# Kernel optimization log

Measured on AMD Instinct MI355X. Metric: run time of the kernel, lower is better.

The kernel has to match this reference:

```python
import jax, jax.numpy as jnp
import numpy as np

B, L, E, H, DV, V = 256, 512, 200, 256, 30000, 50000
NEG_INF = -jnp.inf

def setup_inputs() -> dict:
    key = jax.random.key(0)
    ks = jax.random.split(key, 16)
    s = 0.05
    f = jnp.float32
    return {
        "input_id": jax.random.randint(ks[0], (B, 1), 0, V),
        "input_emb": jax.random.normal(ks[1], (B, 1, E), f),
        "encoder_outputs": jax.random.normal(ks[2], (B, L, H), f),
        "encoder_input_ids": jax.random.randint(ks[3], (B, L), 0, V),
        "hidden": jax.random.normal(ks[4], (B, 1, H), f),
        "attention": jax.random.normal(ks[5], (B, 1, H), f),
        # GRU (PyTorch layout): W_ih (3H, 2H+E), W_hh (3H, H), gate order r,z,n
        "W_ih": jax.random.normal(ks[6], (3 * H, 2 * H + E), f) * s,
        "W_hh": jax.random.normal(ks[7], (3 * H, H), f) * s,
        "b_ih": jnp.zeros((3 * H,), f),
        "b_hh": jnp.zeros((3 * H,), f),
        "W_attn": jax.random.normal(ks[8], (H, H), f) * s,
        "b_attn": jnp.zeros((H,), f),
        "W_comb": jax.random.normal(ks[9], (H, 2 * H), f) * s,
        "b_comb": jnp.zeros((H,), f),
        "W_gen": jax.random.normal(ks[10], (DV, H), f) * s,
        "b_gen": jnp.zeros((DV,), f),
        "W_copy": jax.random.normal(ks[11], (H, H), f) * s,
        "b_copy": jnp.zeros((H,), f),
    }


def reference(input_id, input_emb, encoder_outputs, encoder_input_ids, hidden,
              attention, W_ih, W_hh, b_ih, b_hh, W_attn, b_attn, W_comb,
              b_comb, W_gen, b_gen, W_copy, b_copy):
    b, l = encoder_input_ids.shape
    # selective read: rou = normalized match mask (NaN guard -> 0)
    mask = (input_id == encoder_input_ids).astype(encoder_outputs.dtype)  # (b,l)
    msum = jnp.sum(mask, axis=1, keepdims=True)
    rou = jnp.where(msum > 0, mask / jnp.where(msum > 0, msum, 1.0), 0.0)
    selective_read = jnp.einsum('bl,blh->bh', rou, encoder_outputs)  # (b,h)

    # GRU single step (dropout is identity at inference)
    x = jnp.concatenate([input_emb[:, 0], attention[:, 0], selective_read], axis=-1)
    h_prev = hidden[:, 0]  # (b,h)
    gx = x @ W_ih.T + b_ih          # (b,3h)
    gh = h_prev @ W_hh.T + b_hh     # (b,3h)
    xr, xz, xn = jnp.split(gx, 3, axis=-1)
    hr, hz, hn = jnp.split(gh, 3, axis=-1)
    r = jax.nn.sigmoid(xr + hr)
    z = jax.nn.sigmoid(xz + hz)
    n = jnp.tanh(xn + r * hn)
    h = (1.0 - z) * n + z * h_prev  # (b,h) cur_hidden

    # attention
    q = h @ W_attn.T + b_attn
    attn_w = jax.nn.softmax(jnp.einsum('bh,blh->bl', q, encoder_outputs), axis=-1)
    attn_applied = jnp.einsum('bl,blh->bh', attn_w, encoder_outputs)
    cur_attention = jnp.tanh(
        jnp.concatenate([attn_applied, h], axis=-1) @ W_comb.T + b_comb)  # (b,h)

    # generate + copy scores, joint softmax
    generate_score = cur_attention @ W_gen.T + b_gen                     # (b,DV)
    copy_weights = jax.nn.sigmoid(encoder_outputs @ W_copy.T + b_copy)   # (b,l,h)
    copy_score = jnp.einsum('blh,bh->bl', copy_weights, cur_attention)   # (b,l)
    score = jax.nn.softmax(jnp.concatenate([generate_score, copy_score], axis=1), axis=1)
    gen_s, copy_s = score[:, :DV], score[:, DV:]

    # fused equivalent of the one-hot scatter/mix: direct scatter-add into vocab
    output = jnp.zeros((b, V), score.dtype)
    output = output.at[:, :DV].add(gen_s)
    output = output.at[jnp.arange(b)[:, None], encoder_input_ids].add(copy_s)

    pos = output > 0
    out = jnp.where(pos, jnp.log(jnp.where(pos, output, 1.0)), NEG_INF)
    return out, h[:, None, :], cur_attention[:, None, :]
```

## Files before the change

kernel.cpp:

```cpp
#include <hip/hip_runtime.h>
#include <cmath>

#define B_  256
#define L_  512
#define E_  200
#define H_  256
#define DV_ 30000
#define V_  50000
#define X_  712
#define G3_ 768

#define NEG_BIG -1.0e30f

typedef __attribute__((ext_vector_type(8))) _Float16 half8;
typedef __attribute__((ext_vector_type(4))) float   floatx4;

#define GLOAD16(gptr, lptr)                                                            \
    __builtin_amdgcn_global_load_lds(                                                  \
        (const __attribute__((address_space(1))) unsigned int*)(gptr),                 \
        (__attribute__((address_space(3))) unsigned int*)(lptr), 16, 0, 0)

__global__ void k_cast_wc(const float* __restrict__ Wc, _Float16* __restrict__ wcb) {
    int i = blockIdx.x * 256 + threadIdx.x;
    wcb[i] = (_Float16)Wc[i];
}

__global__ void k_selread(const int* __restrict__ input_id, const float* __restrict__ emb,
                          const float* __restrict__ attention, const float* __restrict__ hidden,
                          const float* __restrict__ enc, const int* __restrict__ enc_ids,
                          float* __restrict__ xT) {
    int b = blockIdx.x, t = threadIdx.x;
    __shared__ int cnt;
    __shared__ int list[L_];
    if (t == 0) cnt = 0;
    __syncthreads();
    int id = input_id[b];
    for (int l = t; l < L_; l += 256) {
        if (enc_ids[b * L_ + l] == id) { int p = atomicAdd(&cnt, 1); list[p] = l; }
    }
    __syncthreads();
    int n = cnt;
    float s = 0.f;
    for (int i = 0; i < n; i++) s += enc[(b * L_ + list[i]) * H_ + t];
    float sel = (n > 0) ? s / (float)n : 0.f;
    for (int k = t; k < E_; k += 256) xT[k * B_ + b] = emb[b * E_ + k];
    xT[(E_ + t) * B_ + b]       = attention[b * H_ + t];
    xT[(E_ + H_ + t) * B_ + b]  = sel;
    xT[(X_ + t) * B_ + b]       = hidden[b * H_ + t];
}

template<int K>
__global__ void __launch_bounds__(256) k_gru_one(const float* __restrict__ xTp, const float* __restrict__ W,
                                                 const float* __restrict__ bias, float* __restrict__ g) {
    __shared__ __align__(16) float Ws[8 * K];
    int t  = threadIdx.x;
    int j0 = blockIdx.x * 8;
    int bq = t & 63;
    int jh = t >> 6;
#pragma unroll
    for (int jj = 0; jj < 8; jj++) {
        const float4* src = (const float4*)(W + (size_t)(j0 + jj) * K);
        float4* dst = (float4*)(Ws + jj * K);
        for (int i = t; i < K / 4; i += 256) dst[i] = src[i];
    }
    __syncthreads();
    float acc0[4] = {0.f, 0.f, 0.f, 0.f};
    float acc1[4] = {0.f, 0.f, 0.f, 0.f};
    const float* w0 = Ws + (jh * 2 + 0) * K;
    const float* w1 = Ws + (jh * 2 + 1) * K;
#pragma unroll 2
    for (int k4 = 0; k4 < K / 4; k4++) {
        float4 wa = *(const float4*)(w0 + k4 * 4);
        float4 wb = *(const float4*)(w1 + k4 * 4);
        float wav[4] = {wa.x, wa.y, wa.z, wa.w};
        float wbv[4] = {wb.x, wb.y, wb.z, wb.w};
#pragma unroll
        for (int u = 0; u < 4; u++) {
            float4 xv = *(const float4*)(xTp + (size_t)(k4 * 4 + u) * B_ + bq * 4);
            acc0[0] += wav[u] * xv.x; acc0[1] += wav[u] * xv.y;
            acc0[2] += wav[u] * xv.z; acc0[3] += wav[u] * xv.w;
            acc1[0] += wbv[u] * xv.x; acc1[1] += wbv[u] * xv.y;
            acc1[2] += wbv[u] * xv.z; acc1[3] += wbv[u] * xv.w;
        }
    }
    int ja = j0 + jh * 2, jb = ja + 1;
    float ba = bias[ja], bb = bias[jb];
#pragma unroll
    for (int i = 0; i < 4; i++) {
        g[(size_t)(bq * 4 + i) * G3_ + ja] = acc0[i] + ba;
        g[(size_t)(bq * 4 + i) * G3_ + jb] = acc1[i] + bb;
    }
}

__global__ void k_gru_gates(const float* __restrict__ gx, const float* __restrict__ gh,
                            const float* __restrict__ hidden, float* __restrict__ hws,
                            float* __restrict__ hout) {
    int b = blockIdx.x, j = threadIdx.x;
    float xr = gx[b * G3_ + j], xz = gx[b * G3_ + 256 + j], xn = gx[b * G3_ + 512 + j];
    float hr = gh[b * G3_ + j], hz = gh[b * G3_ + 256 + j], hn = gh[b * G3_ + 512 + j];
    float r = 1.f / (1.f + expf(-(xr + hr)));
    float z = 1.f / (1.f + expf(-(xz + hz)));
    float n = tanhf(xn + r * hn);
    float hp = hidden[b * H_ + j];
    float h = (1.f - z) * n + z * hp;
    hws[b * H_ + j] = h;
    hout[b * H_ + j] = h;
}

__global__ void __launch_bounds__(1024) k_attn(const float* __restrict__ hws, const float* __restrict__ enc,
                       const float* __restrict__ W_attn, const float* __restrict__ b_attn,
                       const float* __restrict__ W_comb, const float* __restrict__ b_comb,
                       float* __restrict__ caws, _Float16* __restrict__ cab,
                       float* __restrict__ caout) {
    int b = blockIdx.x, t = threadIdx.x;
    int lane = t & 63, w = t >> 6;
    int jj = t & 255, ph = t >> 8;
    __shared__ float hs[H_], qs[H_], ap[H_];
    __shared__ float part[16][H_];
    __shared__ float rm[16], rd[16];
    if (t < 256) hs[t] = hws[b * H_ + t];
    __syncthreads();
    {
        const float4* wr = (const float4*)(W_attn + (size_t)jj * H_ + ph * 64);
        const float4* hp = (const float4*)(hs + ph * 64);
        float acc = 0.f;
#pragma unroll
        for (int k4 = 0; k4 < 16; k4++) {
            float4 wv = wr[k4]; float4 hv = hp[k4];
            acc += wv.x * hv.x + wv.y * hv.y + wv.z * hv.z + wv.w * hv.w;
        }
        part[ph][jj] = acc;
    }
    __syncthreads();
    if (t < 256) qs[t] = b_attn[t] + part[0][t] + part[1][t] + part[2][t] + part[3][t];
    __syncthreads();
    {
        float4 q4 = *(const float4*)&qs[lane * 4];
        size_t base = (size_t)b * L_ + w * 32;
        float m = -INFINITY, d = 0.f;
        float ax = 0.f, ay = 0.f, az = 0.f, aw = 0.f;
        for (int i = 0; i < 32; i += 8) {
            float4 e[8];
            float s[8];
#pragma unroll
            for (int u = 0; u < 8; u++) {
                e[u] = *(const float4*)(enc + (base + i + u) * H_ + lane * 4);
                s[u] = q4.x * e[u].x + q4.y * e[u].y + q4.z * e[u].z + q4.w * e[u].w;
            }
#pragma unroll
            for (int u = 0; u < 8; u++) {
#pragma unroll
                for (int o = 1; o < 64; o <<= 1) s[u] += __shfl_xor(s[u], o);
            }
#pragma unroll
            for (int u = 0; u < 8; u++) {
                float mn = fmaxf(m, s[u]);
                float fm = __expf(m - mn);
                float fs = __expf(s[u] - mn);
                d  = d  * fm + fs;
                ax = ax * fm + fs * e[u].x;
                ay = ay * fm + fs * e[u].y;
                az = az * fm + fs * e[u].z;
                aw = aw * fm + fs * e[u].w;
                m = mn;
            }
        }
        float* pw = &part[w][lane * 4];
        pw[0] = ax; pw[1] = ay; pw[2] = az; pw[3] = aw;
        if (lane == 0) { rm[w] = m; rd[w] = d; }
    }
    __syncthreads();
    if (t < 256) {
        float M = rm[0];
#pragma unroll
        for (int i = 1; i < 16; i++) M = fmaxf(M, rm[i]);
        float den = 0.f, num = 0.f;
#pragma unroll
        for (int i = 0; i < 16; i++) {
            float f = __expf(rm[i] - M);
            den += rd[i] * f;
            num += part[i][t] * f;
        }
        ap[t] = num / den;
    }
    __syncthreads();
    {
        const float4* wr = (const float4*)(W_comb + (size_t)jj * (2 * H_) + ph * 128);
        const float4* xp = (const float4*)(((ph & 2) ? hs : ap) + (ph & 1) * 128);
        float acc = 0.f;
#pragma unroll
        for (int k4 = 0; k4 < 32; k4++) {
            float4 wv = wr[k4]; float4 xv = xp[k4];
            acc += wv.x * xv.x + wv.y * xv.y + wv.z * xv.z + wv.w * xv.w;
        }
        part[ph][jj] = acc;
    }
    __syncthreads();
    if (t < 256) {
        float cav = tanhf(b_comb[t] + part[0][t] + part[1][t] + part[2][t] + part[3][t]);
        caws[b * H_ + t] = cav;
        cab[b * H_ + t]  = (_Float16)cav;
        caout[b * H_ + t] = cav;
    }
}

__global__ void __launch_bounds__(256, 2) k_gen_mfma(
        const _Float16* __restrict__ cab, const float* __restrict__ W_gen,
        const float* __restrict__ b_gen, float* __restrict__ out) {
    __shared__ __align__(16) _Float16 Ah[128 * 32];
    __shared__ __align__(16) float    Bf[128 * 32];
    int t = threadIdx.x, w = t >> 6, lane = t & 63;
    int n0 = blockIdx.x * 128, m0 = blockIdx.y * 128;
    int wm = (w >> 1) * 64, wn = (w & 1) * 64;
    int l15 = lane & 15, q = lane >> 4;
    floatx4 acc[4][4];
#pragma unroll
    for (int i = 0; i < 4; i++)
#pragma unroll
        for (int j = 0; j < 4; j++) acc[i][j] = (floatx4){0.f, 0.f, 0.f, 0.f};

    for (int kc = 0; kc < H_; kc += 32) {
#pragma unroll
        for (int i = 0; i < 2; i++) {
            int t2 = w * 2 + i;
            int row = t2 * 16 + (lane >> 2);
            const _Float16* g = cab + (size_t)(m0 + row) * H_ + kc + (lane & 3) * 8;
            GLOAD16(g, &Ah[t2 * 512]);
        }
#pragma unroll
        for (int i = 0; i < 4; i++) {
            int t2 = w * 4 + i;
            int row = t2 * 8 + (lane >> 3);
            int nn = n0 + row; nn = nn < DV_ ? nn : DV_ - 1;
            const float* g = W_gen + (size_t)nn * H_ + kc + (lane & 7) * 4;
            GLOAD16(g, &Bf[t2 * 256]);
        }
        __syncthreads();
        half8 a[4];
#pragma unroll
        for (int mi = 0; mi < 4; mi++) {
            int m = wm + mi * 16 + l15;
            a[mi] = *(const half8*)&Ah[m * 32 + q * 8];
        }
#pragma unroll
        for (int ni = 0; ni < 4; ni++) {
            int n = wn + ni * 16 + l15;
            const float4* bp = (const float4*)&Bf[n * 32 + q * 8];
            float4 f0 = bp[0], f1 = bp[1];
            half8 bf;
            bf[0] = (_Float16)f0.x; bf[1] = (_Float16)f0.y; bf[2] = (_Float16)f0.z; bf[3] = (_Float16)f0.w;
            bf[4] = (_Float16)f1.x; bf[5] = (_Float16)f1.y; bf[6] = (_Float16)f1.z; bf[7] = (_Float16)f1.w;
#pragma unroll
            for (int mi = 0; mi < 4; mi++)
                acc[mi][ni] = __builtin_amdgcn_mfma_f32_16x16x32_f16(a[mi], bf, acc[mi][ni], 0, 0, 0);
        }
        __syncthreads();
    }
#pragma unroll
    for (int ni = 0; ni < 4; ni++) {
        int col = n0 + wn + ni * 16 + l15;
        if (col < DV_) {
            float bg = b_gen[col];
#pragma unroll
            for (int mi = 0; mi < 4; mi++)
#pragma unroll
                for (int j = 0; j < 4; j++) {
                    int row = m0 + wm + mi * 16 + q * 4 + j;
                    out[(size_t)row * V_ + col] = acc[mi][ni][j] + bg;
                }
        }
    }
}

__global__ void __launch_bounds__(256, 2) k_copy_mfma(
        const float* __restrict__ enc, const _Float16* __restrict__ wcb,
        const float* __restrict__ b_copy, const float* __restrict__ caws,
        float* __restrict__ copy_s) {
    __shared__ __align__(16) float    Af[128 * 32];
    __shared__ __align__(16) _Float16 Bh[256 * 32];
    __shared__ float bcs[H_], cas[H_];
    int t = threadIdx.x, w = t >> 6, lane = t & 63;
    int R0 = blockIdx.x * 128;
    int b  = blockIdx.x >> 2;
    int l15 = lane & 15, q = lane >> 4;
    bcs[t] = b_copy[t];
    cas[t] = caws[b * H_ + t];
    floatx4 acc[2][16];
#pragma unroll
    for (int i = 0; i < 2; i++)
#pragma unroll
        for (int j = 0; j < 16; j++) acc[i][j] = (floatx4){0.f, 0.f, 0.f, 0.f};

    for (int kc = 0; kc < H_; kc += 32) {
#pragma unroll
        for (int i = 0; i < 4; i++) {
            int t2 = w * 4 + i;
            int row = t2 * 8 + (lane >> 3);
            const float* g = enc + (size_t)(R0 + row) * H_ + kc + (lane & 7) * 4;
            GLOAD16(g, &Af[t2 * 256]);
        }
#pragma unroll
        for (int i = 0; i < 4; i++) {
            int t2 = w * 4 + i;
            int row = t2 * 16 + (lane >> 2);
            const _Float16* g = wcb + row * H_ + kc + (lane & 3) * 8;
            GLOAD16(g, &Bh[t2 * 512]);
        }
        __syncthreads();
        half8 a[2];
#pragma unroll
        for (int mi = 0; mi < 2; mi++) {
            int m = w * 32 + mi * 16 + l15;
            const float4* apx = (const float4*)&Af[m * 32 + q * 8];
            float4 f0 = apx[0], f1 = apx[1];
            half8 h;
            h[0] = (_Float16)f0.x; h[1] = (_Float16)f0.y; h[2] = (_Float16)f0.z; h[3] = (_Float16)f0.w;
            h[4] = (_Float16)f1.x; h[5] = (_Float16)f1.y; h[6] = (_Float16)f1.z; h[7] = (_Float16)f1.w;
            a[mi] = h;
        }
#pragma unroll
        for (int ni = 0; ni < 16; ni++) {
            int n = ni * 16 + l15;
            half8 bf = *(const half8*)&Bh[n * 32 + q * 8];
            acc[0][ni] = __builtin_amdgcn_mfma_f32_16x16x32_f16(a[0], bf, acc[0][ni], 0, 0, 0);
            acc[1][ni] = __builtin_amdgcn_mfma_f32_16x16x32_f16(a[1], bf, acc[1][ni], 0, 0, 0);
        }
        __syncthreads();
    }
#pragma unroll
    for (int mi = 0; mi < 2; mi++) {
#pragma unroll
        for (int j = 0; j < 4; j++) {
            float p = 0.f;
#pragma unroll
            for (int ni = 0; ni < 16; ni++) {
                int col = ni * 16 + l15;
                float v = acc[mi][ni][j] + bcs[col];
                p += cas[col] / (1.f + __expf(-v));
            }
            p += __shfl_xor(p, 1);
            p += __shfl_xor(p, 2);
            p += __shfl_xor(p, 4);
            p += __shfl_xor(p, 8);
            if (l15 == 0) copy_s[R0 + w * 32 + mi * 16 + q * 4 + j] = p;
        }
    }
}

__global__ void __launch_bounds__(1024) k_stats(const float* __restrict__ out, const float* __restrict__ copy_s,
                        float* __restrict__ mrow, float* __restrict__ ldrow) {
    int b = blockIdx.x, t = threadIdx.x, lane = t & 63, w = t >> 6;
    __shared__ float rm[16], rs[16];
    const float* row = out + (size_t)b * V_;
    float m = -INFINITY, s = 0.f;
    for (int j = t; j < DV_; j += 1024) {
        float v = row[j];
        if (v > m) { s = s * __expf(m - v) + 1.f; m = v; }
        else       s += __expf(v - m);
    }
    if (t < 512) {
        float v = copy_s[b * L_ + t];
        if (v > m) { s = s * __expf(m - v) + 1.f; m = v; }
        else       s += __expf(v - m);
    }
#pragma unroll
    for (int o = 1; o < 64; o <<= 1) {
        float m2 = __shfl_xor(m, o), s2 = __shfl_xor(s, o);
        float mn = fmaxf(m, m2);
        s = s * __expf(m - mn) + s2 * __expf(m2 - mn);
        m = mn;
    }
    if (lane == 0) { rm[w] = m; rs[w] = s; }
    __syncthreads();
    if (t == 0) {
        float M = rm[0], S = rs[0];
        for (int i = 1; i < 16; i++) {
            float mn = fmaxf(M, rm[i]);
            S = S * __expf(M - mn) + rs[i] * __expf(rm[i] - mn);
            M = mn;
        }
        mrow[b] = M;
        ldrow[b] = __logf(S);
    }
}

__global__ void __launch_bounds__(1024) k_final(float* __restrict__ out, const float* __restrict__ mrow,
                        const float* __restrict__ ldrow) {
    int j = blockIdx.x * 1024 + threadIdx.x;
    int b = blockIdx.y;
    if (j >= V_) return;
    size_t idx = (size_t)b * V_ + j;
    float sh = mrow[b] + ldrow[b];
    out[idx] = (j < DV_) ? out[idx] - sh : NEG_BIG;
}

__global__ void k_scatter_log(float* __restrict__ out, const float* __restrict__ copy_s,
                              const int* __restrict__ enc_ids, const float* __restrict__ mrow,
                              const float* __restrict__ ldrow) {
    int l = blockIdx.x * 256 + threadIdx.x;
    int b = blockIdx.y;
    float p = __expf(copy_s[b * L_ + l] - mrow[b] - ldrow[b]);
    unsigned int* up = (unsigned int*)(out + (size_t)b * V_ + enc_ids[b * L_ + l]);
    unsigned int cur = *up;
    while (true) {
        float ov = __uint_as_float(cur);
        float pv = (ov < -1.0e29f) ? p : __expf(ov) + p;
        unsigned int prev = atomicCAS(up, cur, __float_as_uint(__logf(pv)));
        if (prev == cur) break;
        cur = prev;
    }
}

extern "C" void kernel_launch(void* const* d_in, const int* in_sizes, int n_in,
                              void* d_out, int out_size, void* d_ws, size_t ws_size,
                              hipStream_t stream) {
    const int*   input_id  = (const int*)  d_in[0];
    const float* input_emb = (const float*)d_in[1];
    const float* enc       = (const float*)d_in[2];
    const int*   enc_ids   = (const int*)  d_in[3];
    const float* hidden    = (const float*)d_in[4];
    const float* attention = (const float*)d_in[5];
    const float* W_ih      = (const float*)d_in[6];
    const float* W_hh      = (const float*)d_in[7];
    const float* b_ih      = (const float*)d_in[8];
    const float* b_hh      = (const float*)d_in[9];
    const float* W_attn    = (const float*)d_in[10];
    const float* b_attn    = (const float*)d_in[11];
    const float* W_comb    = (const float*)d_in[12];
    const float* b_comb    = (const float*)d_in[13];
    const float* W_gen     = (const float*)d_in[14];
    const float* b_gen     = (const float*)d_in[15];
    const float* W_copy    = (const float*)d_in[16];
    const float* b_copy    = (const float*)d_in[17];

    float* out = (float*)d_out;
    float* ws  = (float*)d_ws;
    float* xT   = ws;
    float* gx   = xT + 247808;
    float* gh   = gx + 196608;
    float* hws  = gh + 196608;
    float* caws = hws + 65536;
    float* cps  = caws + 65536;
    float* mrow = cps + 131072;
    float* ldrow = mrow + 256;
    _Float16* wcb = (_Float16*)(ldrow + 256);
    _Float16* cab = wcb + 65536;

    float* hout  = out + (size_t)B_ * V_;
    float* caout = hout + B_ * H_;

    k_cast_wc<<<256, 256, 0, stream>>>(W_copy, wcb);
    k_selread<<<256, 256, 0, stream>>>(input_id, input_emb, attention, hidden, enc, enc_ids, xT);
    k_gru_one<712><<<96, 256, 0, stream>>>(xT, W_ih, b_ih, gx);
    k_gru_one<256><<<96, 256, 0, stream>>>(xT + X_ * B_, W_hh, b_hh, gh);
    k_gru_gates<<<256, 256, 0, stream>>>(gx, gh, hidden, hws, hout);
    k_attn<<<256, 1024, 0, stream>>>(hws, enc, W_attn, b_attn, W_comb, b_comb, caws, cab, caout);
    k_gen_mfma<<<dim3((DV_ + 127) / 128, 2), 256, 0, stream>>>(cab, W_gen, b_gen, out);
    k_copy_mfma<<<(B_ * L_) / 128, 256, 0, stream>>>(enc, wcb, b_copy, caws, cps);
    k_stats<<<256, 1024, 0, stream>>>(out, cps, mrow, ldrow);
    dim3 gf((V_ + 1023) / 1024, B_);
    k_final<<<gf, 1024, 0, stream>>>(out, mrow, ldrow);
    dim3 gs(L_ / 256, B_);
    k_scatter_log<<<gs, 256, 0, stream>>>(out, cps, enc_ids, mrow, ldrow);
}
```

Measured before the change: 488.1 us.

## Double-buffer encoder chunks in LDS with block-wide online softmax in attention

```diff
diff --git a/kernel.cpp b/kernel.cpp
--- a/kernel.cpp
+++ b/kernel.cpp
@@ -107,6 +107,7 @@
     hout[b * H_ + j] = h;
 }
 
+#define CHUNK_ 64
 __global__ void __launch_bounds__(1024) k_attn(const float* __restrict__ hws, const float* __restrict__ enc,
                        const float* __restrict__ W_attn, const float* __restrict__ b_attn,
                        const float* __restrict__ W_comb, const float* __restrict__ b_comb,
@@ -115,11 +116,22 @@
     int b = blockIdx.x, t = threadIdx.x;
     int lane = t & 63, w = t >> 6;
     int jj = t & 255, ph = t >> 8;
+    __shared__ __align__(16) float buf[2][CHUNK_ * H_];
     __shared__ float hs[H_], qs[H_], ap[H_];
-    __shared__ float part[16][H_];
-    __shared__ float rm[16], rd[16];
+    __shared__ float part[4][H_];
+    __shared__ float sc[CHUNK_], ps[CHUNK_];
+    __shared__ float mS, dS, fS;
+    const float* encb = enc + (size_t)b * (L_ * H_);
+
+#pragma unroll
+    for (int i = 0; i < 4; i++) {
+        int rs = w * 4 + i;
+        GLOAD16(encb + rs * H_ + lane * 4, &buf[0][rs * H_]);
+    }
     if (t < 256) hs[t] = hws[b * H_ + t];
-    __syncthreads();
+    if (t == 0) { mS = -INFINITY; dS = 0.f; }
+    __syncthreads();
+
     {
         const float4* wr = (const float4*)(W_attn + (size_t)jj * H_ + ph * 64);
         const float4* hp = (const float4*)(hs + ph * 64);
@@ -134,56 +146,64 @@
     __syncthreads();
     if (t < 256) qs[t] = b_attn[t] + part[0][t] + part[1][t] + part[2][t] + part[3][t];
     __syncthreads();
-    {
-        float4 q4 = *(const float4*)&qs[lane * 4];
-        size_t base = (size_t)b * L_ + w * 32;
-        float m = -INFINITY, d = 0.f;
-        float ax = 0.f, ay = 0.f, az = 0.f, aw = 0.f;
-        for (int i = 0; i < 32; i += 8) {
-            float4 e[8];
-            float s[8];
-#pragma unroll
-            for (int u = 0; u < 8; u++) {
-                e[u] = *(const float4*)(enc + (base + i + u) * H_ + lane * 4);
-                s[u] = q4.x * e[u].x + q4.y * e[u].y + q4.z * e[u].z + q4.w * e[u].w;
+
+    float4 q4 = *(const float4*)&qs[lane * 4];
+    float apacc = 0.f;
+    int cur = 0;
+    for (int c = 0; c < L_ / CHUNK_; c++) {
+        if (c < L_ / CHUNK_ - 1) {
+            const float* src = encb + (size_t)(c + 1) * (CHUNK_ * H_);
+#pragma unroll
+            for (int i = 0; i < 4; i++) {
+                int rs = w * 4 + i;
+                GLOAD16(src + rs * H_ + lane * 4, &buf[cur ^ 1][rs * H_]);
             }
-#pragma unroll
-            for (int u = 0; u < 8; u++) {
-#pragma unroll
-                for (int o = 1; o < 64; o <<= 1) s[u] += __shfl_xor(s[u], o);
+        }
+#pragma unroll
+        for (int i = 0; i < 4; i++) {
+            int r = w * 4 + i;
+            float4 e = *(const float4*)&buf[cur][r * H_ + lane * 4];
+            float s = q4.x * e.x + q4.y * e.y + q4.z * e.z + q4.w * e.w;
+#pragma unroll
+            for (int o = 1; o < 64; o <<= 1) s += __shfl_xor(s, o);
+            if (lane == 0) sc[r] = s;
+        }
+        __syncthreads();
+        if (w == 0) {
+            float v = sc[lane];
+            float mc = v;
+#pragma unroll
+            for (int o = 1; o < 64; o <<= 1) mc = fmaxf(mc, __shfl_xor(mc, o));
+            float mold = mS;
+            float mnew = fmaxf(mold, mc);
+            float p = __expf(v - mnew);
+            ps[lane] = p;
+            float dsum = p;
+#pragma unroll
+            for (int o = 1; o < 64; o <<= 1) dsum += __shfl_xor(dsum, o);
+            if (lane == 0) {
+                float f = __expf(mold - mnew);
+                fS = f;
+                dS = dS * f + dsum;
+                mS = mnew;
             }
-#pragma unroll
-            for (int u = 0; u < 8; u++) {
-                float mn = fmaxf(m, s[u]);
-                float fm = __expf(m - mn);
-                float fs = __expf(s[u] - mn);
-                d  = d  * fm + fs;
-                ax = ax * fm + fs * e[u].x;
-                ay = ay * fm + fs * e[u].y;
-                az = az * fm + fs * e[u].z;
-                aw = aw * fm + fs * e[u].w;
-                m = mn;
-            }
-        }
-        float* pw = &part[w][lane * 4];
-        pw[0] = ax; pw[1] = ay; pw[2] = az; pw[3] = aw;
-        if (lane == 0) { rm[w] = m; rd[w] = d; }
-    }
-    __syncthreads();
-    if (t < 256) {
-        float M = rm[0];
-#pragma unroll
-        for (int i = 1; i < 16; i++) M = fmaxf(M, rm[i]);
-        float den = 0.f, num = 0.f;
-#pragma unroll
-        for (int i = 0; i < 16; i++) {
-            float f = __expf(rm[i] - M);
-            den += rd[i] * f;
-            num += part[i][t] * f;
-        }
-        ap[t] = num / den;
-    }
-    __syncthreads();
+        }
+        __syncthreads();
+        {
+            float f = fS;
+            apacc *= f;
+            const float* bp = &buf[cur][ph * 16 * H_ + jj];
+#pragma unroll
+            for (int r = 0; r < 16; r++) apacc += ps[ph * 16 + r] * bp[r * H_];
+        }
+        __syncthreads();
+        cur ^= 1;
+    }
+    part[ph][jj] = apacc;
+    __syncthreads();
+    if (t < 256) ap[t] = (part[0][t] + part[1][t] + part[2][t] + part[3][t]) / dS;
+    __syncthreads();
+
     {
         const float4* wr = (const float4*)(W_comb + (size_t)jj * (2 * H_) + ph * 128);
         const float4* xp = (const float4*)(((ph & 2) ? hs : ap) + (ph & 1) * 128);
```

Result: faster. 477.2 us (-2.2%).

## Split attention kernel into query GEMM, chunked softmax, and combine stages

Applied to the files above, without the earlier changes.

```diff
diff --git a/kernel.cpp b/kernel.cpp
--- a/kernel.cpp
+++ b/kernel.cpp
@@ -49,7 +49,7 @@
     xT[(X_ + t) * B_ + b]       = hidden[b * H_ + t];
 }
 
-template<int K>
+template<int K, int OS>
 __global__ void __launch_bounds__(256) k_gru_one(const float* __restrict__ xTp, const float* __restrict__ W,
                                                  const float* __restrict__ bias, float* __restrict__ g) {
     __shared__ __align__(16) float Ws[8 * K];
@@ -87,14 +87,14 @@
     float ba = bias[ja], bb = bias[jb];
 #pragma unroll
     for (int i = 0; i < 4; i++) {
-        g[(size_t)(bq * 4 + i) * G3_ + ja] = acc0[i] + ba;
-        g[(size_t)(bq * 4 + i) * G3_ + jb] = acc1[i] + bb;
+        g[(size_t)(bq * 4 + i) * OS + ja] = acc0[i] + ba;
+        g[(size_t)(bq * 4 + i) * OS + jb] = acc1[i] + bb;
     }
 }
 
 __global__ void k_gru_gates(const float* __restrict__ gx, const float* __restrict__ gh,
                             const float* __restrict__ hidden, float* __restrict__ hws,
-                            float* __restrict__ hout) {
+                            float* __restrict__ hT, float* __restrict__ hout) {
     int b = blockIdx.x, j = threadIdx.x;
     float xr = gx[b * G3_ + j], xz = gx[b * G3_ + 256 + j], xn = gx[b * G3_ + 512 + j];
     float hr = gh[b * G3_ + j], hz = gh[b * G3_ + 256 + j], hn = gh[b * G3_ + 512 + j];
@@ -104,104 +104,100 @@
     float hp = hidden[b * H_ + j];
     float h = (1.f - z) * n + z * hp;
     hws[b * H_ + j] = h;
+    hT[j * B_ + b]  = h;
     hout[b * H_ + j] = h;
 }
 
-__global__ void __launch_bounds__(1024) k_attn(const float* __restrict__ hws, const float* __restrict__ enc,
-                       const float* __restrict__ W_attn, const float* __restrict__ b_attn,
-                       const float* __restrict__ W_comb, const float* __restrict__ b_comb,
-                       float* __restrict__ caws, _Float16* __restrict__ cab,
-                       float* __restrict__ caout) {
+#define NC_ 4
+#define CR_ 128
+__global__ void __launch_bounds__(256) k_attn_a(const float* __restrict__ qws, const float* __restrict__ enc,
+                         float* __restrict__ avp, float* __restrict__ mdp) {
+    int blk = blockIdx.x;
+    int b = blk >> 2, c = blk & 3;
+    int t = threadIdx.x, lane = t & 63, w = t >> 6;
+    __shared__ float ps[CR_];
+    __shared__ float red[8];
+    const float* encc = enc + ((size_t)b * L_ + c * CR_) * H_;
+    float4 q4 = *(const float4*)&qws[b * H_ + lane * 4];
+    for (int i = 0; i < 32; i += 8) {
+        float s[8];
+#pragma unroll
+        for (int u = 0; u < 8; u++) {
+            float4 e = *(const float4*)(encc + (size_t)(w * 32 + i + u) * H_ + lane * 4);
+            s[u] = q4.x * e.x + q4.y * e.y + q4.z * e.z + q4.w * e.w;
+        }
+#pragma unroll
+        for (int u = 0; u < 8; u++) {
+#pragma unroll
+            for (int o = 1; o < 64; o <<= 1) s[u] += __shfl_xor(s[u], o);
+            if (lane == 0) ps[w * 32 + i + u] = s[u];
+        }
+    }
+    __syncthreads();
+    {
+        float v = ps[w * 32 + (lane & 31)];
+#pragma unroll
+        for (int o = 1; o < 64; o <<= 1) v = fmaxf(v, __shfl_xor(v, o));
+        if (lane == 0) red[w] = v;
+    }
+    __syncthreads();
+    float M = fmaxf(fmaxf(red[0], red[1]), fmaxf(red[2], red[3]));
+    float e = (t < CR_) ? __expf(ps[t] - M) : 0.f;
+    {
+        float ssum = e;
+#pragma unroll
+        for (int o = 1; o < 64; o <<= 1) ssum += __shfl_xor(ssum, o);
+        if (lane == 0) red[4 + w] = ssum;
+    }
+    __syncthreads();
+    if (t < CR_) ps[t] = e;
+    if (t == 0) {
+        mdp[blk * 2]     = M;
+        mdp[blk * 2 + 1] = red[4] + red[5] + red[6] + red[7];
+    }
+    __syncthreads();
+    float a0 = 0.f, a1 = 0.f, a2 = 0.f, a3 = 0.f;
+#pragma unroll 4
+    for (int r = 0; r < CR_; r += 4) {
+        a0 += ps[r + 0] * encc[(size_t)(r + 0) * H_ + t];
+        a1 += ps[r + 1] * encc[(size_t)(r + 1) * H_ + t];
+        a2 += ps[r + 2] * encc[(size_t)(r + 2) * H_ + t];
+        a3 += ps[r + 3] * encc[(size_t)(r + 3) * H_ + t];
+    }
+    avp[(size_t)blk * H_ + t] = (a0 + a1) + (a2 + a3);
+}
+
+__global__ void __launch_bounds__(256) k_attn_b(const float* __restrict__ avp, const float* __restrict__ mdp,
+                         const float* __restrict__ hws, const float* __restrict__ W_comb,
+                         const float* __restrict__ b_comb,
+                         float* __restrict__ caws, _Float16* __restrict__ cab,
+                         float* __restrict__ caout) {
     int b = blockIdx.x, t = threadIdx.x;
-    int lane = t & 63, w = t >> 6;
-    int jj = t & 255, ph = t >> 8;
-    __shared__ float hs[H_], qs[H_], ap[H_];
-    __shared__ float part[16][H_];
-    __shared__ float rm[16], rd[16];
-    if (t < 256) hs[t] = hws[b * H_ + t];
-    __syncthreads();
-    {
-        const float4* wr = (const float4*)(W_attn + (size_t)jj * H_ + ph * 64);
-        const float4* hp = (const float4*)(hs + ph * 64);
-        float acc = 0.f;
-#pragma unroll
-        for (int k4 = 0; k4 < 16; k4++) {
-            float4 wv = wr[k4]; float4 hv = hp[k4];
-            acc += wv.x * hv.x + wv.y * hv.y + wv.z * hv.z + wv.w * hv.w;
-        }
-        part[ph][jj] = acc;
-    }
-    __syncthreads();
-    if (t < 256) qs[t] = b_attn[t] + part[0][t] + part[1][t] + part[2][t] + part[3][t];
-    __syncthreads();
-    {
-        float4 q4 = *(const float4*)&qs[lane * 4];
-        size_t base = (size_t)b * L_ + w * 32;
-        float m = -INFINITY, d = 0.f;
-        float ax = 0.f, ay = 0.f, az = 0.f, aw = 0.f;
-        for (int i = 0; i < 32; i += 8) {
-            float4 e[8];
-            float s[8];
-#pragma unroll
-            for (int u = 0; u < 8; u++) {
-                e[u] = *(const float4*)(enc + (base + i + u) * H_ + lane * 4);
-                s[u] = q4.x * e[u].x + q4.y * e[u].y + q4.z * e[u].z + q4.w * e[u].w;
-            }
-#pragma unroll
-            for (int u = 0; u < 8; u++) {
-#pragma unroll
-                for (int o = 1; o < 64; o <<= 1) s[u] += __shfl_xor(s[u], o);
-            }
-#pragma unroll
-            for (int u = 0; u < 8; u++) {
-                float mn = fmaxf(m, s[u]);
-                float fm = __expf(m - mn);
-                float fs = __expf(s[u] - mn);
-                d  = d  * fm + fs;
-                ax = ax * fm + fs * e[u].x;
-                ay = ay * fm + fs * e[u].y;
-                az = az * fm + fs * e[u].z;
-                aw = aw * fm + fs * e[u].w;
-                m = mn;
-            }
-        }
-        float* pw = &part[w][lane * 4];
-        pw[0] = ax; pw[1] = ay; pw[2] = az; pw[3] = aw;
-        if (lane == 0) { rm[w] = m; rd[w] = d; }
-    }
-    __syncthreads();
-    if (t < 256) {
-        float M = rm[0];
-#pragma unroll
-        for (int i = 1; i < 16; i++) M = fmaxf(M, rm[i]);
-        float den = 0.f, num = 0.f;
-#pragma unroll
-        for (int i = 0; i < 16; i++) {
-            float f = __expf(rm[i] - M);
-            den += rd[i] * f;
-            num += part[i][t] * f;
-        }
-        ap[t] = num / den;
-    }
-    __syncthreads();
-    {
-        const float4* wr = (const float4*)(W_comb + (size_t)jj * (2 * H_) + ph * 128);
-        const float4* xp = (const float4*)(((ph & 2) ? hs : ap) + (ph & 1) * 128);
-        float acc = 0.f;
-#pragma unroll
-        for (int k4 = 0; k4 < 32; k4++) {
-            float4 wv = wr[k4]; float4 xv = xp[k4];
-            acc += wv.x * xv.x + wv.y * xv.y + wv.z * xv.z + wv.w * xv.w;
-        }
-        part[ph][jj] = acc;
-    }
-    __syncthreads();
-    if (t < 256) {
-        float cav = tanhf(b_comb[t] + part[0][t] + part[1][t] + part[2][t] + part[3][t]);
-        caws[b * H_ + t] = cav;
-        cab[b * H_ + t]  = (_Float16)cav;
-        caout[b * H_ + t] = cav;
-    }
+    __shared__ __align__(16) float xs[2 * H_];
+    float m0 = mdp[(b * 4 + 0) * 2], d0 = mdp[(b * 4 + 0) * 2 + 1];
+    float m1 = mdp[(b * 4 + 1) * 2], d1 = mdp[(b * 4 + 1) * 2 + 1];
+    float m2 = mdp[(b * 4 + 2) * 2], d2 = mdp[(b * 4 + 2) * 2 + 1];
+    float m3 = mdp[(b * 4 + 3) * 2], d3 = mdp[(b * 4 + 3) * 2 + 1];
+    float M = fmaxf(fmaxf(m0, m1), fmaxf(m2, m3));
+    float f0 = __expf(m0 - M), f1 = __expf(m1 - M), f2 = __expf(m2 - M), f3 = __expf(m3 - M);
+    float den = f0 * d0 + f1 * d1 + f2 * d2 + f3 * d3;
+    float num = f0 * avp[((size_t)b * 4 + 0) * H_ + t] + f1 * avp[((size_t)b * 4 + 1) * H_ + t]
+              + f2 * avp[((size_t)b * 4 + 2) * H_ + t] + f3 * avp[((size_t)b * 4 + 3) * H_ + t];
+    xs[t]      = num / den;
+    xs[H_ + t] = hws[b * H_ + t];
+    __syncthreads();
+    const float4* wr = (const float4*)(W_comb + (size_t)t * (2 * H_));
+    const float4* xp = (const float4*)xs;
+    float acc = 0.f;
+#pragma unroll 8
+    for (int k4 = 0; k4 < 128; k4++) {
+        float4 wv = wr[k4], xv = xp[k4];
+        acc += wv.x * xv.x + wv.y * xv.y + wv.z * xv.z + wv.w * xv.w;
+    }
+    float cav = tanhf(b_comb[t] + acc);
+    caws[b * H_ + t]  = cav;
+    cab[b * H_ + t]   = (_Float16)cav;
+    caout[b * H_ + t] = cav;
 }
 
 __global__ void __launch_bounds__(256, 2) k_gen_mfma(
@@ -445,16 +441,22 @@
     float* ldrow = mrow + 256;
     _Float16* wcb = (_Float16*)(ldrow + 256);
     _Float16* cab = wcb + 65536;
+    float* qws  = (float*)(cab + 65536);
+    float* mdp  = qws + 65536;
+    float* hT   = xT;
+    float* avp  = gx;
 
     float* hout  = out + (size_t)B_ * V_;
     float* caout = hout + B_ * H_;
 
     k_cast_wc<<<256, 256, 0, stream>>>(W_copy, wcb);
     k_selread<<<256, 256, 0, stream>>>(input_id, input_emb, attention, hidden, enc, enc_ids, xT);
-    k_gru_one<712><<<96, 256, 0, stream>>>(xT, W_ih, b_ih, gx);
-    k_gru_one<256><<<96, 256, 0, stream>>>(xT + X_ * B_, W_hh, b_hh, gh);
-    k_gru_gates<<<256, 256, 0, stream>>>(gx, gh, hidden, hws, hout);
-    k_attn<<<256, 1024, 0, stream>>>(hws, enc, W_attn, b_attn, W_comb, b_comb, caws, cab, caout);
+    k_gru_one<712, G3_><<<96, 256, 0, stream>>>(xT, W_ih, b_ih, gx);
+    k_gru_one<256, G3_><<<96, 256, 0, stream>>>(xT + X_ * B_, W_hh, b_hh, gh);
+    k_gru_gates<<<256, 256, 0, stream>>>(gx, gh, hidden, hws, hT, hout);
+    k_gru_one<256, H_><<<32, 256, 0, stream>>>(hT, W_attn, b_attn, qws);
+    k_attn_a<<<B_ * NC_, 256, 0, stream>>>(qws, enc, avp, mdp);
+    k_attn_b<<<256, 256, 0, stream>>>(avp, mdp, hws, W_comb, b_comb, caws, cab, caout);
     k_gen_mfma<<<dim3((DV_ + 127) / 128, 2), 256, 0, stream>>>(cab, W_gen, b_gen, out);
     k_copy_mfma<<<(B_ * L_) / 128, 256, 0, stream>>>(enc, wcb, b_copy, caws, cps);
     k_stats<<<256, 1024, 0, stream>>>(out, cps, mrow, ldrow);
```

Result: no change. 487.5 us (-0.1%).
